# Performance work log

Hardware: AMD Instinct MI355X
Metric: run time of the kernel (lower is better)

## Reference

```python
import jax, jax.numpy as jnp
import numpy as np


def conv_gates(x, w, b):
    # x: [B, L, Din]; w: [3O, Din, k]; torch Conv1d with padding=(k-1)//2
    xt = jnp.transpose(x, (0, 2, 1))  # [B, Din, L]
    pad = (w.shape[-1] - 1) // 2
    g = jax.lax.conv_general_dilated(
        xt, w, window_strides=(1,), padding=[(pad, pad)],
        dimension_numbers=('NCH', 'OIH', 'NCH')) + b[None, :, None]
    g = jnp.transpose(g, (0, 2, 1))  # [B, L, 3O]
    f, o, z = jnp.split(g, 3, axis=-1)
    return jax.nn.sigmoid(f), jax.nn.sigmoid(o), jnp.tanh(z)


def fo_pool(f, z):
    # f, z: [B, L, O]; cell_t = f_t * cell_{t-1} + (1 - f_t) * z_t, cell_{-1}=0
    def step(c, fz):
        ft, zt = fz
        c = ft * c + (1.0 - ft) * zt
        return c, c
    c0 = jnp.zeros((f.shape[0], f.shape[2]), f.dtype)
    _, cells = jax.lax.scan(step, c0, (jnp.swapaxes(f, 0, 1), jnp.swapaxes(z, 0, 1)))
    return jnp.swapaxes(cells, 0, 1)  # [B, L, O]


def qrnn_layer(x, wf, bf, wr, br):
    # forward direction
    f, o, z = conv_gates(x, wf, bf)
    cells = fo_pool(f, z)
    hidden = cells * o
    # reverse direction: run recurrence on time-flipped gates, flip back
    fr, orr, zr = conv_gates(x, wr, br)
    rcells = fo_pool(fr[:, ::-1], zr[:, ::-1])[:, ::-1]
    rhidden = rcells * orr
    out = jnp.concatenate([hidden, rhidden], -1)  # [B, L, 2O]
    last_h = jnp.concatenate([hidden[:, -1], rhidden[:, -1]], -1)  # [B, 2O]
    last_c = jnp.concatenate([cells[:, -1], rcells[:, -1]], -1)
    return out, last_h, last_c


def setup_inputs() -> dict:
    key = jax.random.key(0)
    ks = jax.random.split(key, 9)
    D, O, K = 512, 512, 3
    B, L = 16, 2048
    s = 0.05
    return {
        'x': jax.random.normal(ks[0], (B, L, D), jnp.float32),
        'w0f': jax.random.normal(ks[1], (3 * O, D, K), jnp.float32) * s,
        'b0f': jax.random.normal(ks[2], (3 * O,), jnp.float32) * s,
        'w0r': jax.random.normal(ks[3], (3 * O, D, K), jnp.float32) * s,
        'b0r': jax.random.normal(ks[4], (3 * O,), jnp.float32) * s,
        'w1f': jax.random.normal(ks[5], (3 * O, 2 * O, K), jnp.float32) * s,
        'b1f': jax.random.normal(ks[6], (3 * O,), jnp.float32) * s,
        'w1r': jax.random.normal(ks[7], (3 * O, 2 * O, K), jnp.float32) * s,
        'b1r': jax.random.normal(ks[8], (3 * O,), jnp.float32) * s,
    }


def reference(x, w0f, b0f, w0r, b0r, w1f, b1f, w1r, b1r):
    out1, h1, c1 = qrnn_layer(x, w0f, b0f, w0r, b0r)
    out2, h2, c2 = qrnn_layer(out1, w1f, b1f, w1r, b1r)
    B = x.shape[0]
    O = h1.shape[-1] // 2
    # torch: cat along dim 0 -> [2B, 2O] then view(num_dir*num_layers, B, O)
    hidden = jnp.concatenate([h1, h2], 0).reshape(4, B, O)
    cell = jnp.concatenate([c1, c2], 0).reshape(4, B, O)
    return out2, hidden, cell
```

## Files before the change

### kernel.cpp

```cpp
#include <hip/hip_runtime.h>

typedef _Float16 f16x8 __attribute__((ext_vector_type(8)));
typedef float    f32x4 __attribute__((ext_vector_type(4)));

#define GLDS16(gp, lp) \
  __builtin_amdgcn_global_load_lds((const __attribute__((address_space(1))) void*)(gp), \
                                   (__attribute__((address_space(3))) void*)(lp), 16, 0, 0)

#define NB   16
#define LL   2048
#define LP   2050
#define C3   1536
#define OO   512

__global__ void cvt_x_kernel(const float* __restrict__ x, _Float16* __restrict__ xp) {
  int t = blockIdx.x * blockDim.x + threadIdx.x;
  const int total = NB * LP * (512 / 8);
  if (t >= total) return;
  int c8  = (t & 63) << 3;
  int row = t >> 6;
  int b   = row / LP;
  int lp  = row - b * LP;
  f16x8 v;
  if (lp == 0 || lp == LP - 1) {
#pragma unroll
    for (int i = 0; i < 8; ++i) v[i] = (_Float16)0.f;
  } else {
    const float* s = x + ((size_t)(b * LL + lp - 1) * 512 + c8);
    const float4* s4 = (const float4*)s;
    float4 a = s4[0], bq = s4[1];
    v[0] = (_Float16)a.x;  v[1] = (_Float16)a.y;
    v[2] = (_Float16)a.z;  v[3] = (_Float16)a.w;
    v[4] = (_Float16)bq.x; v[5] = (_Float16)bq.y;
    v[6] = (_Float16)bq.z; v[7] = (_Float16)bq.w;
  }
  *(f16x8*)(xp + (size_t)row * 512 + c8) = v;
}

__global__ void cvt_w_kernel(const float* __restrict__ w, _Float16* __restrict__ wt,
                             int Din, int dinsh) {
  int t = blockIdx.x * blockDim.x + threadIdx.x;
  if (t >= C3 * Din) return;
  int c = t >> dinsh;
  int i = t & (Din - 1);
  const float* s = w + (size_t)t * 3;
  wt[((size_t)c * 3 + 0) * Din + i] = (_Float16)s[0];
  wt[((size_t)c * 3 + 1) * Din + i] = (_Float16)s[1];
  wt[((size_t)c * 3 + 2) * Din + i] = (_Float16)s[2];
}

__global__ void zero_pad_kernel(_Float16* __restrict__ xp1) {
  int t = blockIdx.x * blockDim.x + threadIdx.x;
  if (t >= NB * 2 * 1024) return;
  int col = t & 1023;
  int r   = (t >> 10) & 1;
  int b   = t >> 11;
  xp1[((size_t)b * LP + (r ? (LP - 1) : 0)) * 1024 + col] = (_Float16)0.f;
}

__global__ __launch_bounds__(256) void conv_gemm(
    const _Float16* __restrict__ A, const _Float16* __restrict__ W,
    const float* __restrict__ bias, _Float16* __restrict__ G, int Din)
{
  const int nT = blockIdx.x, lT = blockIdx.y, b = blockIdx.z;
  const int tid  = (int)threadIdx.x;
  const int w    = tid >> 6, lane = tid & 63;
  const int wr   = w >> 1,   wc   = w & 1;
  const int l0   = lT << 7,  n0   = nT << 7;

  __shared__ _Float16 Als[128 * 32];
  __shared__ _Float16 Bls[128 * 32];

  f32x4 acc[4][4];
  const f32x4 zed = {0.f, 0.f, 0.f, 0.f};
#pragma unroll
  for (int i = 0; i < 4; ++i)
#pragma unroll
    for (int j = 0; j < 4; ++j) acc[i][j] = zed;

  const int mloc0 = (w << 4) + (lane >> 2);
  const int ke    = (lane & 3) << 3;

  for (int tap = 0; tap < 3; ++tap) {
    const _Float16* Ab = A + ((size_t)(b * LP + l0 + tap)) * Din;
    for (int kt = 0; kt < Din; kt += 32) {
      __syncthreads();
#pragma unroll
      for (int j = 0; j < 2; ++j) {
        const int m     = mloc0 + (j << 6);
        const int chunk = (j << 2) + w;
        GLDS16(Ab + (size_t)m * Din + (kt + ke), (char*)Als + (chunk << 10));
        GLDS16(W + ((size_t)((n0 + m) * 3 + tap)) * Din + (kt + ke),
               (char*)Bls + (chunk << 10));
      }
      __syncthreads();
      f16x8 af[4], bf[4];
      const int rA = lane & 15;
      const int kc = (lane >> 4) << 4;
#pragma unroll
      for (int i = 0; i < 4; ++i) {
        af[i] = *(const f16x8*)((const char*)Als + ((wr * 64 + i * 16 + rA) << 6) + kc);
        bf[i] = *(const f16x8*)((const char*)Bls + ((wc * 64 + i * 16 + rA) << 6) + kc);
      }
#pragma unroll
      for (int mi = 0; mi < 4; ++mi)
#pragma unroll
        for (int ni = 0; ni < 4; ++ni)
          acc[mi][ni] = __builtin_amdgcn_mfma_f32_16x16x32_f16(af[mi], bf[ni], acc[mi][ni], 0, 0, 0);
    }
  }

#pragma unroll
  for (int ni = 0; ni < 4; ++ni) {
    const int col = n0 + wc * 64 + ni * 16 + (lane & 15);
    const float bv = bias[col];
#pragma unroll
    for (int mi = 0; mi < 4; ++mi) {
#pragma unroll
      for (int r = 0; r < 4; ++r) {
        const int l = l0 + wr * 64 + mi * 16 + ((lane >> 4) << 2) + r;
        float v = acc[mi][ni][r] + bv;
        v = fminf(fmaxf(v, -30.f), 30.f);
        float a;
        if (col < 1024) {
          a = 1.f / (1.f + __expf(-v));
        } else {
          float e = __expf(2.f * v);
          a = (e - 1.f) / (e + 1.f);
        }
        G[((size_t)(b * LL + l)) * C3 + col] = (_Float16)a;
      }
    }
  }
}

__global__ void fo_phase1(const _Float16* __restrict__ g, float* __restrict__ P,
                          float* __restrict__ S, int dir) {
  int t = blockIdx.x * blockDim.x + threadIdx.x;
  if (t >= 32 * 8192) return;
  int bo = t & 8191;
  int ch = t >> 13;
  int b = bo >> 9, o = bo & 511;
  float c = 0.f, p = 1.f;
  const int s0 = ch * 64;
  for (int k = 0; k < 64; ++k) {
    int s = s0 + k;
    int l = dir ? (2047 - s) : s;
    size_t base = ((size_t)(b * LL + l)) * C3 + o;
    float f = (float)g[base];
    float z = (float)g[base + 1024];
    c = f * c + (1.f - f) * z;
    p *= f;
  }
  P[t] = p;
  S[t] = c;
}

__global__ void fo_phase2(const float* __restrict__ P, const float* __restrict__ S,
                          float* __restrict__ cst) {
  int bo = blockIdx.x * blockDim.x + threadIdx.x;
  if (bo >= 8192) return;
  float c = 0.f;
#pragma unroll
  for (int j = 0; j < 32; ++j) {
    cst[j * 8192 + bo] = c;
    c = P[j * 8192 + bo] * c + S[j * 8192 + bo];
  }
}

__global__ void fo_phase3(const _Float16* __restrict__ g, const float* __restrict__ cst,
                          int dir, int layer, _Float16* __restrict__ nxt,
                          float* __restrict__ out2, float* __restrict__ hc) {
  int t = blockIdx.x * blockDim.x + threadIdx.x;
  if (t >= 32 * 8192) return;
  int bo = t & 8191;
  int ch = t >> 13;
  int b = bo >> 9, o = bo & 511;
  float c = cst[t];
  const int s0 = ch * 64;
  for (int k = 0; k < 64; ++k) {
    int s = s0 + k;
    int l = dir ? (2047 - s) : s;
    size_t base = ((size_t)(b * LL + l)) * C3 + o;
    float f  = (float)g[base];
    float og = (float)g[base + 512];
    float z  = (float)g[base + 1024];
    c = f * c + (1.f - f) * z;
    float h = c * og;
    if (layer == 0)
      nxt[((size_t)(b * LP + l + 1)) * 1024 + dir * 512 + o] = (_Float16)h;
    else
      out2[((size_t)(b * LL + l)) * 1024 + dir * 512 + o] = h;
    if (l == 2047) {
      hc[(layer * 16 + b) * 1024 + dir * 512 + o] = h;
      hc[32768 + (layer * 16 + b) * 1024 + dir * 512 + o] = c;
    }
  }
}

extern "C" void kernel_launch(void* const* d_in, const int* in_sizes, int n_in,
                              void* d_out, int out_size, void* d_ws, size_t ws_size,
                              hipStream_t stream) {
  const float* x   = (const float*)d_in[0];
  const float* w0f = (const float*)d_in[1];
  const float* b0f = (const float*)d_in[2];
  const float* w0r = (const float*)d_in[3];
  const float* b0r = (const float*)d_in[4];
  const float* w1f = (const float*)d_in[5];
  const float* b1f = (const float*)d_in[6];
  const float* w1r = (const float*)d_in[7];
  const float* b1r = (const float*)d_in[8];
  float* out = (float*)d_out;

  char* ws = (char*)d_ws;
  _Float16* xp0  = (_Float16*)(ws + 0);
  _Float16* xp1  = (_Float16*)(ws + 33587200);
  _Float16* wt0f = (_Float16*)(ws + 100761600);
  _Float16* wt0r = (_Float16*)(ws + 105480192);
  _Float16* wt1f = (_Float16*)(ws + 110198784);
  _Float16* wt1r = (_Float16*)(ws + 119635968);
  _Float16* g    = (_Float16*)(ws + 129073152);
  float*    P    = (float*)(ws + 229736448);
  float*    S    = (float*)(ws + 230785024);
  float*    cst  = (float*)(ws + 231833600);

  float* hc = out + (size_t)16 * 2048 * 1024;

  cvt_x_kernel<<<8200, 256, 0, stream>>>(x, xp0);
  cvt_w_kernel<<<3072, 256, 0, stream>>>(w0f, wt0f, 512, 9);
  cvt_w_kernel<<<3072, 256, 0, stream>>>(w0r, wt0r, 512, 9);
  cvt_w_kernel<<<6144, 256, 0, stream>>>(w1f, wt1f, 1024, 10);
  cvt_w_kernel<<<6144, 256, 0, stream>>>(w1r, wt1r, 1024, 10);
  zero_pad_kernel<<<128, 256, 0, stream>>>(xp1);

  dim3 gg(12, 16, 16);

  conv_gemm<<<gg, 256, 0, stream>>>(xp0, wt0f, b0f, g, 512);
  fo_phase1<<<1024, 256, 0, stream>>>(g, P, S, 0);
  fo_phase2<<<32, 256, 0, stream>>>(P, S, cst);
  fo_phase3<<<1024, 256, 0, stream>>>(g, cst, 0, 0, xp1, out, hc);
  conv_gemm<<<gg, 256, 0, stream>>>(xp0, wt0r, b0r, g, 512);
  fo_phase1<<<1024, 256, 0, stream>>>(g, P, S, 1);
  fo_phase2<<<32, 256, 0, stream>>>(P, S, cst);
  fo_phase3<<<1024, 256, 0, stream>>>(g, cst, 1, 0, xp1, out, hc);
  conv_gemm<<<gg, 256, 0, stream>>>(xp1, wt1f, b1f, g, 1024);
  fo_phase1<<<1024, 256, 0, stream>>>(g, P, S, 0);
  fo_phase2<<<32, 256, 0, stream>>>(P, S, cst);
  fo_phase3<<<1024, 256, 0, stream>>>(g, cst, 0, 1, xp1, out, hc);
  conv_gemm<<<gg, 256, 0, stream>>>(xp1, wt1r, b1r, g, 1024);
  fo_phase1<<<1024, 256, 0, stream>>>(g, P, S, 1);
  fo_phase2<<<32, 256, 0, stream>>>(P, S, cst);
  fo_phase3<<<1024, 256, 0, stream>>>(g, cst, 1, 1, xp1, out, hc);
}
```

Measured before the change: 1.735 ms.

## Share A tile across conv taps and XOR-swizzle LDS layout in conv GEMM

Restructures the conv GEMM loop so each K-slice loads a 132-row A tile once and all three tap weight tiles, then computes the three taps from shifted rows of the same A tile. This removes the redundant reloading of activations for each tap and cuts the number of barrier pairs by three. It also XOR-swizzles the 16-byte column chunks in LDS to reduce bank conflicts on fragment reads. LDS use per block grows, which may lower occupancy.

New measurement: 1.426 ms. 17.8% less time.

```diff
diff --git a/kernel.cpp b/kernel.cpp
--- a/kernel.cpp
+++ b/kernel.cpp
@@ -68,8 +68,8 @@
   const int wr   = w >> 1,   wc   = w & 1;
   const int l0   = lT << 7,  n0   = nT << 7;
 
-  __shared__ _Float16 Als[128 * 32];
-  __shared__ _Float16 Bls[128 * 32];
+  __shared__ _Float16 Als[132 * 32];
+  __shared__ _Float16 Bls[3 * 128 * 32];
 
   f32x4 acc[4][4];
   const f32x4 zed = {0.f, 0.f, 0.f, 0.f};
@@ -78,29 +78,44 @@
 #pragma unroll
     for (int j = 0; j < 4; ++j) acc[i][j] = zed;
 
-  const int mloc0 = (w << 4) + (lane >> 2);
-  const int ke    = (lane & 3) << 3;
-
-  for (int tap = 0; tap < 3; ++tap) {
-    const _Float16* Ab = A + ((size_t)(b * LP + l0 + tap)) * Din;
-    for (int kt = 0; kt < Din; kt += 32) {
-      __syncthreads();
-#pragma unroll
-      for (int j = 0; j < 2; ++j) {
-        const int m     = mloc0 + (j << 6);
-        const int chunk = (j << 2) + w;
-        GLDS16(Ab + (size_t)m * Din + (kt + ke), (char*)Als + (chunk << 10));
-        GLDS16(W + ((size_t)((n0 + m) * 3 + tap)) * Din + (kt + ke),
-               (char*)Bls + (chunk << 10));
-      }
-      __syncthreads();
+  const int rl   = lane >> 2;
+  const int kswz = ((lane & 3) ^ (rl & 3)) << 3;
+  const _Float16* Ab = A + ((size_t)(b * LP + l0)) * Din;
+
+  const int rA = lane & 15;
+  const int kq = lane >> 4;
+
+  for (int kt = 0; kt < Din; kt += 32) {
+    __syncthreads();
+#pragma unroll
+    for (int j = 0; j < 2; ++j) {
+      const int chunk = w + (j << 2);
+      const int row   = (chunk << 4) + rl;
+      GLDS16(Ab + (size_t)row * Din + (kt + kswz), (char*)Als + (chunk << 10));
+    }
+    if (w == 0 && lane < 8) {
+      const int row = 128 + rl;
+      GLDS16(Ab + (size_t)row * Din + (kt + kswz), (char*)Als + (8 << 10));
+    }
+#pragma unroll
+    for (int j = 0; j < 6; ++j) {
+      const int chunkid = w * 6 + j;
+      const int tap     = chunkid >> 3;
+      const int row     = ((chunkid & 7) << 4) + rl;
+      GLDS16(W + ((size_t)((n0 + row) * 3 + tap)) * Din + (kt + kswz),
+             (char*)Bls + (chunkid << 10));
+    }
+    __syncthreads();
+
+#pragma unroll
+    for (int tap = 0; tap < 3; ++tap) {
       f16x8 af[4], bf[4];
-      const int rA = lane & 15;
-      const int kc = (lane >> 4) << 4;
 #pragma unroll
       for (int i = 0; i < 4; ++i) {
-        af[i] = *(const f16x8*)((const char*)Als + ((wr * 64 + i * 16 + rA) << 6) + kc);
-        bf[i] = *(const f16x8*)((const char*)Bls + ((wc * 64 + i * 16 + rA) << 6) + kc);
+        const int ra = wr * 64 + i * 16 + rA + tap;
+        const int rb = wc * 64 + i * 16 + rA;
+        af[i] = *(const f16x8*)((const char*)Als + (ra << 6) + ((kq ^ (ra & 3)) << 4));
+        bf[i] = *(const f16x8*)((const char*)Bls + (tap << 13) + (rb << 6) + ((kq ^ (rb & 3)) << 4));
       }
 #pragma unroll
       for (int mi = 0; mi < 4; ++mi)
```
